# Kernel optimization log

Measured on AMD Instinct MI355X. Metric: run time of the kernel, lower is better.

The kernel has to match this reference:

```python
import jax, jax.numpy as jnp
import numpy as np

B, CIN, COUT, K, H, W = 4, 16, 16, 3, 128, 128


def setup_inputs() -> dict:
    key = jax.random.key(0)
    k1, k2, k3 = jax.random.split(key, 3)
    x = jax.random.normal(k1, (B, CIN, H, W), dtype=jnp.float32)
    # kaiming_uniform_(a=1.0): bound = sqrt(6 / ((1 + a^2) * fan_in)), fan_in = Cin*k*k
    fan_in = CIN * K * K
    bound = float(np.sqrt(6.0 / (2.0 * fan_in)))
    weights = jax.random.uniform(k2, (H, W, COUT, CIN, K, K), dtype=jnp.float32,
                                 minval=-bound, maxval=bound)
    bias = jax.random.normal(k3, (H, W, COUT), dtype=jnp.float32)
    return {"x": x, "weights": weights, "bias": bias}


def _xonv2d(x, weights, bias):
    b, c, h, w = x.shape
    k = weights.shape[-1]
    pad = k // 2
    if k % 2 == 1:
        xp = jnp.pad(x, ((0, 0), (0, 0), (pad, pad), (pad, pad)))
    else:
        xp = jnp.pad(x, ((0, 0), (0, 0), (pad - 1, pad), (pad - 1, pad)))
    # Unfold: patch element order matches torch view -> (c, kh, kw) flattened.
    # Stack k*k shifted views: (B, C, k*k, H, W)
    shifts = [xp[:, :, i:i + h, j:j + w] for i in range(k) for j in range(k)]
    patches = jnp.stack(shifts, axis=2)
    wflat = weights.reshape(h, w, weights.shape[2], c, k * k)  # (H,W,O,C,p)
    # out[b,o,h,w] = sum_{c,p} patches[b,c,p,h,w] * wflat[h,w,o,c,p]
    out = jnp.einsum('bcphw,hwocp->bohw', patches, wflat)
    out = out + jnp.transpose(bias, (2, 0, 1))[None]  # (1,O,H,W)
    return out


def reference(x, weights, bias):
    return _xonv2d(x, weights, bias)
```

## Files before the change

### kernel.cpp

```cpp
#include <hip/hip_runtime.h>


#define HWD   128
#define CIND  16
#define COUTD 16
#define BATCH 4
#define SPW   8
#define WPB   4

typedef float f4  __attribute__((ext_vector_type(4)));
typedef float f4u __attribute__((ext_vector_type(4), aligned(4)));

__device__ __forceinline__ void gload_lds16(const f4* gsrc, f4* ldst) {
    __builtin_amdgcn_global_load_lds(
        (const __attribute__((address_space(1))) unsigned int*)gsrc,
        (__attribute__((address_space(3))) unsigned int*)ldst,
        16, 0, 0);
}

__global__ __launch_bounds__(256) void xonv2d_kernel(
    const float* __restrict__ x,
    const float* __restrict__ wts,
    const float* __restrict__ bias,
    float* __restrict__ out)
{
    __shared__ f4 wsm[WPB][2][576];

    const int lane = threadIdx.x & 63;
    const int wave = threadIdx.x >> 6;

    const int xcd = blockIdx.x & 7;
    const int idx = blockIdx.x >> 3;
    const int site0 = xcd * 2048 + (idx * WPB + wave) * SPW;

    const int o  = lane & 15;
    const int g  = lane >> 4;
    const int c0 = g * 4;

    {
        const f4* gw = (const f4*)wts + (size_t)site0 * 576;
        #pragma unroll
        for (int j = 0; j < 9; ++j)
            gload_lds16(gw + j * 64 + lane, &wsm[wave][0][j * 64]);
        gw += 576;
        #pragma unroll
        for (int j = 0; j < 9; ++j)
            gload_lds16(gw + j * 64 + lane, &wsm[wave][1][j * 64]);
    }

    #pragma unroll 1
    for (int s = 0; s < SPW; ++s) {
        const int site = site0 + s;
        const int h = site >> 7;
        const int w = site & 127;

        if (s < SPW - 1) asm volatile("s_waitcnt vmcnt(9)" ::: "memory");
        else             asm volatile("s_waitcnt vmcnt(0)" ::: "memory");

        const float bv = bias[(size_t)site * COUTD + o];

        f4 wv[9];
        {
            const f4* lp = &wsm[wave][s & 1][o * 36 + g * 9];
            #pragma unroll
            for (int j = 0; j < 9; ++j) wv[j] = lp[j];
        }
        const float* wf = (const float*)wv;

        float acc[BATCH] = {0.f, 0.f, 0.f, 0.f};

        const bool interior = (h >= 1) & (h <= HWD - 2) & (w >= 1) & (w <= HWD - 3);

        if (interior) {
            #pragma unroll
            for (int cc = 0; cc < 4; ++cc) {
                #pragma unroll
                for (int b = 0; b < BATCH; ++b) {
                    const float* xb = x + (((size_t)(b * CIND + c0 + cc) * HWD + (h - 1)) * HWD) + (w - 1);
                    f4 r0 = *(const f4u*)(xb);
                    f4 r1 = *(const f4u*)(xb + HWD);
                    f4 r2 = *(const f4u*)(xb + 2 * HWD);
                    const float* wr = wf + cc * 9;
                    acc[b] = fmaf(r0.x, wr[0], acc[b]);
                    acc[b] = fmaf(r0.y, wr[1], acc[b]);
                    acc[b] = fmaf(r0.z, wr[2], acc[b]);
                    acc[b] = fmaf(r1.x, wr[3], acc[b]);
                    acc[b] = fmaf(r1.y, wr[4], acc[b]);
                    acc[b] = fmaf(r1.z, wr[5], acc[b]);
                    acc[b] = fmaf(r2.x, wr[6], acc[b]);
                    acc[b] = fmaf(r2.y, wr[7], acc[b]);
                    acc[b] = fmaf(r2.z, wr[8], acc[b]);
                }
            }
        } else {
            #pragma unroll
            for (int cc = 0; cc < 4; ++cc) {
                #pragma unroll
                for (int b = 0; b < BATCH; ++b) {
                    const float* xb = x + ((size_t)(b * CIND + c0 + cc)) * (HWD * HWD);
                    #pragma unroll
                    for (int kh = 0; kh < 3; ++kh) {
                        const int hy = h + kh - 1;
                        #pragma unroll
                        for (int kw = 0; kw < 3; ++kw) {
                            const int wx = w + kw - 1;
                            const bool ok = (hy >= 0) & (hy < HWD) & (wx >= 0) & (wx < HWD);
                            const float xv = ok ? xb[hy * HWD + wx] : 0.f;
                            acc[b] = fmaf(xv, wf[cc * 9 + kh * 3 + kw], acc[b]);
                        }
                    }
                }
            }
        }

        float r[BATCH];
        #pragma unroll
        for (int b = 0; b < BATCH; ++b) {
            float v = acc[b];
            v += __shfl_xor(v, 32);
            v += __shfl_xor(v, 16);
            r[b] = v;
        }

        const float vout = (g == 0) ? r[0] : (g == 1) ? r[1] : (g == 2) ? r[2] : r[3];
        out[((size_t)(g * COUTD + o)) * (HWD * HWD) + h * HWD + w] = vout + bv;

        if (s + 2 < SPW) {
            __builtin_amdgcn_sched_barrier(0);
            const f4* gw = (const f4*)wts + (size_t)(site + 2) * 576;
            #pragma unroll
            for (int j = 0; j < 9; ++j)
                gload_lds16(gw + j * 64 + lane, &wsm[wave][s & 1][j * 64]);
            __builtin_amdgcn_sched_barrier(0);
        }
    }
}

extern "C" void kernel_launch(void* const* d_in, const int* in_sizes, int n_in,
                              void* d_out, int out_size, void* d_ws, size_t ws_size,
                              hipStream_t stream) {
    const float* x    = (const float*)d_in[0];
    const float* wts  = (const float*)d_in[1];
    const float* bias = (const float*)d_in[2];
    float* out = (float*)d_out;

    const int blocks = (HWD * HWD) / (WPB * SPW);
    xonv2d_kernel<<<blocks, WPB * 64, 0, stream>>>(x, wts, bias, out);
}
```

Measured before the change: 239.4 us.

## Stage input patches cooperatively in LDS and single-buffer weight prefetch

Each wave now loads the 4x16x3 input row segments for its site once, spread across lanes, stages them in shared memory, and all lanes read from there. Before, the 16 output-channel lanes sharing a channel group each issued the same global loads. The weight double buffer becomes a single buffer. The next site's weights are prefetched right after the current weights move into registers. Sites per wave are halved, which doubles the block count. This trades redundant global/L1 traffic and the interior/border branch for an extra LDS round trip, and it gives less prefetch distance for the dominant weight stream.

```diff
diff --git a/kernel.cpp b/kernel.cpp
--- a/kernel.cpp
+++ b/kernel.cpp
@@ -5,7 +5,7 @@
 #define CIND  16
 #define COUTD 16
 #define BATCH 4
-#define SPW   8
+#define SPW   4
 #define WPB   4
 
 typedef float f4  __attribute__((ext_vector_type(4)));
@@ -24,7 +24,8 @@
     const float* __restrict__ bias,
     float* __restrict__ out)
 {
-    __shared__ f4 wsm[WPB][2][576];
+    __shared__ f4 wbuf[WPB][576];
+    __shared__ f4 xslot[WPB][192];
 
     const int lane = threadIdx.x & 63;
     const int wave = threadIdx.x >> 6;
@@ -37,15 +38,21 @@
     const int g  = lane >> 4;
     const int c0 = g * 4;
 
+    int sb[3], sc[3], sr[3];
+    #pragma unroll
+    for (int j = 0; j < 3; ++j) {
+        const int S = lane + 64 * j;
+        sb[j] = S / 48;
+        const int u = S - sb[j] * 48;
+        sc[j] = u / 3;
+        sr[j] = u - sc[j] * 3;
+    }
+
     {
         const f4* gw = (const f4*)wts + (size_t)site0 * 576;
         #pragma unroll
         for (int j = 0; j < 9; ++j)
-            gload_lds16(gw + j * 64 + lane, &wsm[wave][0][j * 64]);
-        gw += 576;
-        #pragma unroll
-        for (int j = 0; j < 9; ++j)
-            gload_lds16(gw + j * 64 + lane, &wsm[wave][1][j * 64]);
+            gload_lds16(gw + j * 64 + lane, &wbuf[wave][j * 64]);
     }
 
     #pragma unroll 1
@@ -54,62 +61,80 @@
         const int h = site >> 7;
         const int w = site & 127;
 
-        if (s < SPW - 1) asm volatile("s_waitcnt vmcnt(9)" ::: "memory");
-        else             asm volatile("s_waitcnt vmcnt(0)" ::: "memory");
-
-        const float bv = bias[(size_t)site * COUTD + o];
+        if (s == 0) asm volatile("s_waitcnt vmcnt(0)" ::: "memory");
+        else        asm volatile("s_waitcnt vmcnt(1)" ::: "memory");
+        __builtin_amdgcn_sched_barrier(0);
 
         f4 wv[9];
         {
-            const f4* lp = &wsm[wave][s & 1][o * 36 + g * 9];
+            const f4* lp = &wbuf[wave][o * 36 + g * 9];
             #pragma unroll
             for (int j = 0; j < 9; ++j) wv[j] = lp[j];
         }
+        asm volatile("s_waitcnt lgkmcnt(0)" ::: "memory");
+        __builtin_amdgcn_sched_barrier(0);
         const float* wf = (const float*)wv;
 
+        f4 xr[3];
+        const bool wfast = (w >= 1) && (w <= HWD - 3);
+        #pragma unroll
+        for (int j = 0; j < 3; ++j) {
+            const int hy  = h + sr[j] - 1;
+            const bool okh = (unsigned)hy < (unsigned)HWD;
+            const int hyc = okh ? hy : 0;
+            const float* xb = x + ((size_t)(sb[j] * CIND + sc[j]) * HWD + hyc) * HWD;
+            if (wfast) {
+                f4 v = *(const f4u*)(xb + (w - 1));
+                xr[j] = okh ? v : (f4){0.f, 0.f, 0.f, 0.f};
+            } else {
+                f4 v;
+                #pragma unroll
+                for (int jj = 0; jj < 4; ++jj) {
+                    const int cw = w - 1 + jj;
+                    const bool ok = okh && ((unsigned)cw < (unsigned)HWD);
+                    v[jj] = ok ? xb[cw] : 0.f;
+                }
+                xr[j] = v;
+            }
+        }
+        const float bv = bias[(size_t)site * COUTD + o];
+        __builtin_amdgcn_sched_barrier(0);
+
+        if (s + 1 < SPW) {
+            const f4* gw = (const f4*)wts + (size_t)(site + 1) * 576;
+            #pragma unroll
+            for (int j = 0; j < 9; ++j)
+                gload_lds16(gw + j * 64 + lane, &wbuf[wave][j * 64]);
+        }
+        __builtin_amdgcn_sched_barrier(0);
+
+        if (s + 1 < SPW) asm volatile("s_waitcnt vmcnt(9)" ::: "memory");
+        else             asm volatile("s_waitcnt vmcnt(0)" ::: "memory");
+        __builtin_amdgcn_sched_barrier(0);
+
+        #pragma unroll
+        for (int j = 0; j < 3; ++j)
+            xslot[wave][lane + 64 * j] = xr[j];
+
         float acc[BATCH] = {0.f, 0.f, 0.f, 0.f};
-
-        const bool interior = (h >= 1) & (h <= HWD - 2) & (w >= 1) & (w <= HWD - 3);
-
-        if (interior) {
+        #pragma unroll
+        for (int cc = 0; cc < 4; ++cc) {
             #pragma unroll
-            for (int cc = 0; cc < 4; ++cc) {
-                #pragma unroll
-                for (int b = 0; b < BATCH; ++b) {
-                    const float* xb = x + (((size_t)(b * CIND + c0 + cc) * HWD + (h - 1)) * HWD) + (w - 1);
-                    f4 r0 = *(const f4u*)(xb);
-                    f4 r1 = *(const f4u*)(xb + HWD);
-                    f4 r2 = *(const f4u*)(xb + 2 * HWD);
-                    const float* wr = wf + cc * 9;
-                    acc[b] = fmaf(r0.x, wr[0], acc[b]);
-                    acc[b] = fmaf(r0.y, wr[1], acc[b]);
-                    acc[b] = fmaf(r0.z, wr[2], acc[b]);
-                    acc[b] = fmaf(r1.x, wr[3], acc[b]);
-                    acc[b] = fmaf(r1.y, wr[4], acc[b]);
-                    acc[b] = fmaf(r1.z, wr[5], acc[b]);
-                    acc[b] = fmaf(r2.x, wr[6], acc[b]);
-                    acc[b] = fmaf(r2.y, wr[7], acc[b]);
-                    acc[b] = fmaf(r2.z, wr[8], acc[b]);
-                }
-            }
-        } else {
-            #pragma unroll
-            for (int cc = 0; cc < 4; ++cc) {
-                #pragma unroll
-                for (int b = 0; b < BATCH; ++b) {
-                    const float* xb = x + ((size_t)(b * CIND + c0 + cc)) * (HWD * HWD);
-                    #pragma unroll
-                    for (int kh = 0; kh < 3; ++kh) {
-                        const int hy = h + kh - 1;
-                        #pragma unroll
-                        for (int kw = 0; kw < 3; ++kw) {
-                            const int wx = w + kw - 1;
-                            const bool ok = (hy >= 0) & (hy < HWD) & (wx >= 0) & (wx < HWD);
-                            const float xv = ok ? xb[hy * HWD + wx] : 0.f;
-                            acc[b] = fmaf(xv, wf[cc * 9 + kh * 3 + kw], acc[b]);
-                        }
-                    }
-                }
+            for (int b = 0; b < BATCH; ++b) {
+                const f4* xp = &xslot[wave][(b * CIND + c0 + cc) * 3];
+                const f4 r0 = xp[0];
+                const f4 r1 = xp[1];
+                const f4 r2 = xp[2];
+                const float* wr = wf + cc * 9;
+                acc[b] = fmaf(r0.x, wr[0], acc[b]);
+                acc[b] = fmaf(r0.y, wr[1], acc[b]);
+                acc[b] = fmaf(r0.z, wr[2], acc[b]);
+                acc[b] = fmaf(r1.x, wr[3], acc[b]);
+                acc[b] = fmaf(r1.y, wr[4], acc[b]);
+                acc[b] = fmaf(r1.z, wr[5], acc[b]);
+                acc[b] = fmaf(r2.x, wr[6], acc[b]);
+                acc[b] = fmaf(r2.y, wr[7], acc[b]);
+                acc[b] = fmaf(r2.z, wr[8], acc[b]);
             }
         }
 
@@ -124,15 +149,6 @@
 
         const float vout = (g == 0) ? r[0] : (g == 1) ? r[1] : (g == 2) ? r[2] : r[3];
         out[((size_t)(g * COUTD + o)) * (HWD * HWD) + h * HWD + w] = vout + bv;
-
-        if (s + 2 < SPW) {
-            __builtin_amdgcn_sched_barrier(0);
-            const f4* gw = (const f4*)wts + (size_t)(site + 2) * 576;
-            #pragma unroll
-            for (int j = 0; j < 9; ++j)
-                gload_lds16(gw + j * 64 + lane, &wsm[wave][s & 1][j * 64]);
-            __builtin_amdgcn_sched_barrier(0);
-        }
     }
 }
 
```

Result: no change. 240.6 us (+0.5%).

## Stage input halo tile in LDS and single-buffer weight prefetch with vectorized stores

Applied to the files above, without the earlier changes.

Each block now cooperatively loads a zero-padded 3-row halo tile of x (all batches and channels) into shared memory, so the inner loop reads activations from LDS with no interior/boundary branching. Weight staging changes from a double-buffered LDS ring to a single buffer: weights are copied to registers, then the next site's prefetch is issued. Bias is preloaded, and the 8 per-site outputs are gathered into registers and written as two float4 stores. The aim is to cut redundant global x reads and uncoalesced scalar stores, at the cost of a block-wide barrier, more LDS, and shorter weight prefetch lookahead.

```diff
diff --git a/kernel.cpp b/kernel.cpp
--- a/kernel.cpp
+++ b/kernel.cpp
@@ -4,9 +4,9 @@
 #define HWD   128
 #define CIND  16
 #define COUTD 16
-#define BATCH 4
 #define SPW   8
 #define WPB   4
+#define XROWF 44
 
 typedef float f4  __attribute__((ext_vector_type(4)));
 typedef float f4u __attribute__((ext_vector_type(4), aligned(4)));
@@ -24,116 +24,113 @@
     const float* __restrict__ bias,
     float* __restrict__ out)
 {
-    __shared__ f4 wsm[WPB][2][576];
+    __shared__ float xs[192 * XROWF];
+    __shared__ f4 wbuf[WPB][576];
 
-    const int lane = threadIdx.x & 63;
-    const int wave = threadIdx.x >> 6;
+    const int tid  = threadIdx.x;
+    const int lane = tid & 63;
+    const int wv   = tid >> 6;
 
-    const int xcd = blockIdx.x & 7;
-    const int idx = blockIdx.x >> 3;
-    const int site0 = xcd * 2048 + (idx * WPB + wave) * SPW;
+    const int xcd  = blockIdx.x & 7;
+    const int idx  = blockIdx.x >> 3;
+    const int sblk = xcd * 2048 + idx * 32;
+    const int h    = sblk >> 7;
+    const int w0b  = sblk & 127;
+    const int w0   = w0b + wv * 8;
 
     const int o  = lane & 15;
     const int g  = lane >> 4;
     const int c0 = g * 4;
 
-    {
-        const f4* gw = (const f4*)wts + (size_t)site0 * 576;
-        #pragma unroll
-        for (int j = 0; j < 9; ++j)
-            gload_lds16(gw + j * 64 + lane, &wsm[wave][0][j * 64]);
-        gw += 576;
-        #pragma unroll
-        for (int j = 0; j < 9; ++j)
-            gload_lds16(gw + j * 64 + lane, &wsm[wave][1][j * 64]);
+    #pragma unroll
+    for (int j = 0; j < 8; ++j) {
+        const int t = tid + 256 * j;
+        if (t < 1920) {
+            const int R = t / 10, q = t - R * 10;
+            const int b = R / 48;
+            const int u = R - b * 48;
+            const int c = u / 3, r = u - c * 3;
+            const int hy = h + r - 1;
+            const int cb = w0b - 4 + 4 * q;
+            f4 v = {0.f, 0.f, 0.f, 0.f};
+            if (((unsigned)hy < (unsigned)HWD) & ((unsigned)cb <= (unsigned)(HWD - 4)))
+                v = *(const f4u*)(x + ((size_t)(b * CIND + c) * HWD + hy) * HWD + cb);
+            *(f4*)&xs[R * XROWF + q * 4] = v;
+        }
     }
 
-    #pragma unroll 1
+    float bvr[SPW];
+    #pragma unroll
+    for (int s = 0; s < SPW; ++s)
+        bvr[s] = bias[(size_t)(sblk + wv * 8 + s) * COUTD + o];
+
+    const f4* gw0 = (const f4*)wts + (size_t)(sblk + wv * 8) * 576;
+    #pragma unroll
+    for (int j = 0; j < 9; ++j)
+        gload_lds16(gw0 + j * 64 + lane, &wbuf[wv][j * 64]);
+
+    __syncthreads();
+
+    f4 rsA, rsB;
+
+    #pragma unroll
     for (int s = 0; s < SPW; ++s) {
-        const int site = site0 + s;
-        const int h = site >> 7;
-        const int w = site & 127;
+        if (s > 0) asm volatile("s_waitcnt vmcnt(0)" ::: "memory");
+        __builtin_amdgcn_sched_barrier(0);
 
-        if (s < SPW - 1) asm volatile("s_waitcnt vmcnt(9)" ::: "memory");
-        else             asm volatile("s_waitcnt vmcnt(0)" ::: "memory");
+        f4 wvr[9];
+        {
+            const f4* lp = &wbuf[wv][o * 36 + g * 9];
+            #pragma unroll
+            for (int j = 0; j < 9; ++j) wvr[j] = lp[j];
+        }
+        asm volatile("s_waitcnt lgkmcnt(0)" ::: "memory");
+        __builtin_amdgcn_sched_barrier(0);
 
-        const float bv = bias[(size_t)site * COUTD + o];
+        if (s + 1 < SPW) {
+            const f4* gw = gw0 + (size_t)(s + 1) * 576;
+            #pragma unroll
+            for (int j = 0; j < 9; ++j)
+                gload_lds16(gw + j * 64 + lane, &wbuf[wv][j * 64]);
+        }
+        __builtin_amdgcn_sched_barrier(0);
 
-        f4 wv[9];
-        {
-            const f4* lp = &wsm[wave][s & 1][o * 36 + g * 9];
+        const float* wf = (const float*)wvr;
+        const int slot0 = wv * 8 + s + 3;
+        float acc[4] = {0.f, 0.f, 0.f, 0.f};
+        #pragma unroll
+        for (int cc = 0; cc < 4; ++cc) {
             #pragma unroll
-            for (int j = 0; j < 9; ++j) wv[j] = lp[j];
-        }
-        const float* wf = (const float*)wv;
-
-        float acc[BATCH] = {0.f, 0.f, 0.f, 0.f};
-
-        const bool interior = (h >= 1) & (h <= HWD - 2) & (w >= 1) & (w <= HWD - 3);
-
-        if (interior) {
-            #pragma unroll
-            for (int cc = 0; cc < 4; ++cc) {
+            for (int b = 0; b < 4; ++b) {
                 #pragma unroll
-                for (int b = 0; b < BATCH; ++b) {
-                    const float* xb = x + (((size_t)(b * CIND + c0 + cc) * HWD + (h - 1)) * HWD) + (w - 1);
-                    f4 r0 = *(const f4u*)(xb);
-                    f4 r1 = *(const f4u*)(xb + HWD);
-                    f4 r2 = *(const f4u*)(xb + 2 * HWD);
-                    const float* wr = wf + cc * 9;
-                    acc[b] = fmaf(r0.x, wr[0], acc[b]);
-                    acc[b] = fmaf(r0.y, wr[1], acc[b]);
-                    acc[b] = fmaf(r0.z, wr[2], acc[b]);
-                    acc[b] = fmaf(r1.x, wr[3], acc[b]);
-                    acc[b] = fmaf(r1.y, wr[4], acc[b]);
-                    acc[b] = fmaf(r1.z, wr[5], acc[b]);
-                    acc[b] = fmaf(r2.x, wr[6], acc[b]);
-                    acc[b] = fmaf(r2.y, wr[7], acc[b]);
-                    acc[b] = fmaf(r2.z, wr[8], acc[b]);
-                }
-            }
-        } else {
-            #pragma unroll
-            for (int cc = 0; cc < 4; ++cc) {
-                #pragma unroll
-                for (int b = 0; b < BATCH; ++b) {
-                    const float* xb = x + ((size_t)(b * CIND + c0 + cc)) * (HWD * HWD);
-                    #pragma unroll
-                    for (int kh = 0; kh < 3; ++kh) {
-                        const int hy = h + kh - 1;
-                        #pragma unroll
-                        for (int kw = 0; kw < 3; ++kw) {
-                            const int wx = w + kw - 1;
-                            const bool ok = (hy >= 0) & (hy < HWD) & (wx >= 0) & (wx < HWD);
-                            const float xv = ok ? xb[hy * HWD + wx] : 0.f;
-                            acc[b] = fmaf(xv, wf[cc * 9 + kh * 3 + kw], acc[b]);
-                        }
-                    }
+                for (int r = 0; r < 3; ++r) {
+                    const int R = (b * CIND + c0 + cc) * 3 + r;
+                    const float* xp = &xs[R * XROWF + slot0];
+                    const float* wr = wf + cc * 9 + r * 3;
+                    acc[b] = fmaf(xp[0], wr[0], acc[b]);
+                    acc[b] = fmaf(xp[1], wr[1], acc[b]);
+                    acc[b] = fmaf(xp[2], wr[2], acc[b]);
                 }
             }
         }
 
-        float r[BATCH];
+        float rr[4];
         #pragma unroll
-        for (int b = 0; b < BATCH; ++b) {
+        for (int b = 0; b < 4; ++b) {
             float v = acc[b];
             v += __shfl_xor(v, 32);
             v += __shfl_xor(v, 16);
-            r[b] = v;
+            rr[b] = v;
         }
+        const float vout = (g == 0) ? rr[0] : (g == 1) ? rr[1]
+                         : (g == 2) ? rr[2] : rr[3];
+        const float ov = vout + bvr[s];
+        if (s < 4) rsA[s] = ov; else rsB[s - 4] = ov;
+    }
 
-        const float vout = (g == 0) ? r[0] : (g == 1) ? r[1] : (g == 2) ? r[2] : r[3];
-        out[((size_t)(g * COUTD + o)) * (HWD * HWD) + h * HWD + w] = vout + bv;
-
-        if (s + 2 < SPW) {
-            __builtin_amdgcn_sched_barrier(0);
-            const f4* gw = (const f4*)wts + (size_t)(site + 2) * 576;
-            #pragma unroll
-            for (int j = 0; j < 9; ++j)
-                gload_lds16(gw + j * 64 + lane, &wsm[wave][s & 1][j * 64]);
-            __builtin_amdgcn_sched_barrier(0);
-        }
-    }
+    float* ob = out + ((size_t)(g * COUTD + o)) * (HWD * HWD) + h * HWD + w0;
+    *(f4*)(ob)     = rsA;
+    *(f4*)(ob + 4) = rsB;
 }
 
 extern "C" void kernel_launch(void* const* d_in, const int* in_sizes, int n_in,
```

New measurement: 229.0 us. -4.3%, faster.
